# Optimization experiments

Measured on AMD Instinct MI355X. Metric: run time of the kernel, lower is better.

## Reference

```python
import jax, jax.numpy as jnp
import numpy as np

B, D, Nh, L = 8, 128, 8, 1024
Dk = D // Nh  # 16
Dv = D // Nh  # 16

def _xavier(key, shape):
    # nn.init.xavier_normal_ on a 3D tensor treats dim0 as fan irrelevant:
    # fan_in = shape[-1]*1, fan_out = shape[-2]*1 for >=2D; receptive field = prod(shape[2:])? For 3D torch uses
    # fan_in = shape[1]*shape[2]? We just need same distribution family; use std from last two dims.
    fan_in, fan_out = shape[-1], shape[-2]
    std = float(np.sqrt(2.0 / (fan_in + fan_out)))
    return jax.random.normal(key, shape, dtype=jnp.float32) * std

def setup_inputs() -> dict:
    key = jax.random.key(0)
    kx, kq, kk, kv, ko = jax.random.split(key, 5)
    x = jax.random.normal(kx, (B, D, L), dtype=jnp.float32)
    Wq = _xavier(kq, (Nh, B, Dk, D))
    Wk = _xavier(kk, (Nh, B, Dk, D))
    Wv = _xavier(kv, (Nh, B, Dv, D))
    Wo = _xavier(ko, (B, Dv * Nh, D))
    return {"x": x, "Wq": Wq, "Wk": Wk, "Wv": Wv, "Wo": Wo}

def reference(x, Wq, Wk, Wv, Wo):
    scale = 1.0 / np.sqrt(Dk)
    # Project all heads at once: [Nh,B,Dk,D] x [B,D,L] -> [B,Nh,Dk,L]
    Q = jnp.einsum('hbkd,bdl->bhkl', Wq, x)
    K = jnp.einsum('hbkd,bdl->bhkl', Wk, x)
    V = jnp.einsum('hbvd,bdl->bhvl', Wv, x)
    # scores[b,h,i,j] = sum_k Q[b,h,k,i] * K[b,h,k,j]
    scores = jnp.einsum('bhki,bhkj->bhij', Q, K) * scale
    # original softmaxes over dim=1 of [B,L,L] -> the i (Q-length) axis
    attn = jax.nn.softmax(scores, axis=2)
    # head[b,h,v,j] = sum_i V[b,h,v,i] * attn[b,h,i,j]
    head = jnp.einsum('bhvi,bhij->bhvj', V, attn)
    # concat heads along channel dim (order matches torch.cat over head list)
    head = head.reshape(B, Nh * Dv, L)
    # Wo [B, Nh*Dv, D] bmm head [B, D(=Nh*Dv), L] -> [B, Nh*Dv, L]
    out = jnp.einsum('bod,bdl->bol', Wo, head)
    return out
```

## Files before the change

kernel.cpp:

```cpp
#include <hip/hip_runtime.h>
#include <hip/hip_bf16.h>

#define B_ 8
#define D_ 128
#define NH 8
#define L_ 1024
#define DK 16

typedef __attribute__((ext_vector_type(4))) short s4;
typedef __attribute__((ext_vector_type(4))) float f4;

static __device__ __forceinline__ unsigned short f2bf(float f) {
    __hip_bfloat16 h = __float2bfloat16(f);
    return *reinterpret_cast<unsigned short*>(&h);
}
static __device__ __forceinline__ unsigned pack2(float a, float b) {
    return (unsigned)f2bf(a) | ((unsigned)f2bf(b) << 16);
}
static __device__ __forceinline__ s4 pack4(float a, float b, float c, float d) {
    union { unsigned u[2]; s4 v; } un;
    un.u[0] = pack2(a, b);
    un.u[1] = pack2(c, d);
    return un.v;
}

#if __has_builtin(__builtin_amdgcn_mfma_f32_16x16x16_bf16)
#define MFMA16(a, b, c) __builtin_amdgcn_mfma_f32_16x16x16_bf16(a, b, c, 0, 0, 0)
#elif __has_builtin(__builtin_amdgcn_mfma_f32_16x16x16bf16_1k)
#define MFMA16(a, b, c) __builtin_amdgcn_mfma_f32_16x16x16bf16_1k(a, b, c, 0, 0, 0)
#else
static __device__ __forceinline__ f4 mfma16_asm(s4 a, s4 b, f4 c) {
    f4 d;
    asm volatile("v_mfma_f32_16x16x16_bf16 %0, %1, %2, %3"
                 : "=&v"(d) : "v"(a), "v"(b), "v"(c));
    return d;
}
#define MFMA16(a, b, c) mfma16_asm(a, b, c)
#endif

__global__ __launch_bounds__(256)
void proj_kernel(const float* __restrict__ x,
                 const float* __restrict__ Wq,
                 const float* __restrict__ Wk,
                 const float* __restrict__ Wv,
                 unsigned short* __restrict__ Qt,
                 unsigned short* __restrict__ Kt,
                 unsigned short* __restrict__ Vt) {
    const int lane = threadIdx.x & 63;
    const int wv   = threadIdx.x >> 6;
    const int m = lane & 15, q = lane >> 4;
    const int bh = blockIdx.y, b = bh >> 3, h = bh & 7;
    const int which = blockIdx.z;
    const int n0 = (blockIdx.x * 4 + wv) * 32;

    const float* W = (which == 0) ? Wq : (which == 1) ? Wk : Wv;
    const float* Wrow = W + ((size_t)((h * B_ + b) * DK + m)) * D_;
    const float* xb = x + (size_t)b * D_ * L_ + n0 + m;

    f4 acc0 = {0.f, 0.f, 0.f, 0.f}, acc1 = {0.f, 0.f, 0.f, 0.f};
#pragma unroll
    for (int kb = 0; kb < 8; ++kb) {
        const int k4 = kb * 16 + q * 4;
        float4 wf = *(const float4*)(Wrow + k4);
        s4 a = pack4(wf.x, wf.y, wf.z, wf.w);

        const float* xc = xb + (size_t)k4 * L_;
        float b00 = xc[0];          float b01 = xc[L_];
        float b02 = xc[2 * L_];     float b03 = xc[3 * L_];
        float b10 = xc[16];         float b11 = xc[L_ + 16];
        float b12 = xc[2 * L_ + 16];float b13 = xc[3 * L_ + 16];
        s4 bf0 = pack4(b00, b01, b02, b03);
        s4 bf1 = pack4(b10, b11, b12, b13);

        acc0 = MFMA16(a, bf0, acc0);
        acc1 = MFMA16(a, bf1, acc1);
    }

    if (which == 2) {
        unsigned short* vp = Vt + ((size_t)bh * DK + q * 4) * L_ + n0 + m;
        vp[0]      = f2bf(acc0[0]); vp[L_]     = f2bf(acc0[1]);
        vp[2 * L_] = f2bf(acc0[2]); vp[3 * L_] = f2bf(acc0[3]);
        vp += 16;
        vp[0]      = f2bf(acc1[0]); vp[L_]     = f2bf(acc1[1]);
        vp[2 * L_] = f2bf(acc1[2]); vp[3 * L_] = f2bf(acc1[3]);
    } else {
        const float sc = (which == 1) ? 0.25f : 1.0f;
        unsigned short* T = (which == 0) ? Qt : Kt;
        uint2 u0, u1;
        u0.x = pack2(acc0[0] * sc, acc0[1] * sc);
        u0.y = pack2(acc0[2] * sc, acc0[3] * sc);
        u1.x = pack2(acc1[0] * sc, acc1[1] * sc);
        u1.y = pack2(acc1[2] * sc, acc1[3] * sc);
        *(uint2*)(T + ((size_t)bh * L_ + n0 + m) * DK + q * 4)      = u0;
        *(uint2*)(T + ((size_t)bh * L_ + n0 + 16 + m) * DK + q * 4) = u1;
    }
}

__global__ __launch_bounds__(256)
void attn_mfma_kernel(const unsigned short* __restrict__ Qt,
                      const unsigned short* __restrict__ Kt,
                      const unsigned short* __restrict__ Vt,
                      unsigned short* __restrict__ headT) {
    const int lane = threadIdx.x & 63;
    const int wv   = threadIdx.x >> 6;
    const int m    = lane & 15;
    const int q    = lane >> 4;
    const int jt   = blockIdx.x * 4 + wv;
    const int j0   = jt * 16;
    const int bh   = blockIdx.y, b = bh >> 3, h = bh & 7;

    s4 bk = *(const s4*)(Kt + ((size_t)bh * L_ + j0 + m) * DK + q * 4);

    f4 O = {0.f, 0.f, 0.f, 0.f};
    float ls = 0.f;
    const unsigned short* qbase = Qt + (size_t)bh * L_ * DK + q * 4;
    const unsigned short* vbase = Vt + ((size_t)bh * DK + m) * L_ + q * 4;

#pragma unroll 4
    for (int i0 = 0; i0 < L_; i0 += 16) {
        s4 aq = *(const s4*)(qbase + (size_t)(i0 + m) * DK);
        s4 av = *(const s4*)(vbase + i0);

        f4 z = {0.f, 0.f, 0.f, 0.f};
        f4 S = MFMA16(aq, bk, z);

        float p0 = __expf(S[0]), p1 = __expf(S[1]);
        float p2 = __expf(S[2]), p3 = __expf(S[3]);
        ls += (p0 + p1) + (p2 + p3);

        s4 pb;
        pb[0] = (short)f2bf(p0); pb[1] = (short)f2bf(p1);
        pb[2] = (short)f2bf(p2); pb[3] = (short)f2bf(p3);

        O = MFMA16(av, pb, O);
    }

    ls += __shfl_xor(ls, 16, 64);
    ls += __shfl_xor(ls, 32, 64);
    const float inv = 1.f / ls;

    uint2 o;
    o.x = pack2(O[0] * inv, O[1] * inv);
    o.y = pack2(O[2] * inv, O[3] * inv);
    *(uint2*)(headT + ((size_t)b * L_ + j0 + m) * D_ + h * DK + q * 4) = o;
}

__global__ __launch_bounds__(256)
void out_kernel(const unsigned short* __restrict__ headT,
                const float* __restrict__ Wo,
                float* __restrict__ out) {
    const int lane = threadIdx.x & 63;
    const int wv   = threadIdx.x >> 6;
    const int m = lane & 15, q = lane >> 4;
    const int task = blockIdx.x * 4 + wv;
    const int oc = task >> 5;
    const int n0 = (task & 31) * 32;
    const int b  = blockIdx.y;
    const int o0 = oc * 16;

    const float* Wrow = Wo + ((size_t)b * D_ + o0 + m) * D_;
    const unsigned short* h0 = headT + ((size_t)b * L_ + n0 + m) * D_;
    const unsigned short* h1 = h0 + 16 * D_;

    f4 acc0 = {0.f, 0.f, 0.f, 0.f}, acc1 = {0.f, 0.f, 0.f, 0.f};
#pragma unroll
    for (int kb = 0; kb < 8; ++kb) {
        const int k4 = kb * 16 + q * 4;
        float4 wf = *(const float4*)(Wrow + k4);
        s4 a  = pack4(wf.x, wf.y, wf.z, wf.w);
        s4 b0 = *(const s4*)(h0 + k4);
        s4 b1 = *(const s4*)(h1 + k4);
        acc0 = MFMA16(a, b0, acc0);
        acc1 = MFMA16(a, b1, acc1);
    }

    float* op = out + ((size_t)b * D_ + o0 + q * 4) * L_ + n0 + m;
    op[0]      = acc0[0]; op[L_]     = acc0[1];
    op[2 * L_] = acc0[2]; op[3 * L_] = acc0[3];
    op += 16;
    op[0]      = acc1[0]; op[L_]     = acc1[1];
    op[2 * L_] = acc1[2]; op[3 * L_] = acc1[3];
}

extern "C" void kernel_launch(void* const* d_in, const int* in_sizes, int n_in,
                              void* d_out, int out_size, void* d_ws, size_t ws_size,
                              hipStream_t stream) {
    const float* x  = (const float*)d_in[0];
    const float* Wq = (const float*)d_in[1];
    const float* Wk = (const float*)d_in[2];
    const float* Wv = (const float*)d_in[3];
    const float* Wo = (const float*)d_in[4];
    float* out = (float*)d_out;

    const size_t SEG = (size_t)B_ * NH * DK * L_;
    unsigned short* Qt    = (unsigned short*)d_ws;
    unsigned short* Kt    = Qt + SEG;
    unsigned short* Vt    = Kt + SEG;
    unsigned short* headT = Vt + SEG;

    proj_kernel<<<dim3(8, B_ * NH, 3),  256, 0, stream>>>(x, Wq, Wk, Wv, Qt, Kt, Vt);
    attn_mfma_kernel<<<dim3(16, B_ * NH), 256, 0, stream>>>(Qt, Kt, Vt, headT);
    out_kernel <<<dim3(64, B_),         256, 0, stream>>>(headT, Wo, out);
}
```

Before: 119.6 us.

## Fuse attention with output projection via shared-memory head tile

Merges the attention kernel and the output-projection kernel into one kernel. Each block computes a 32-column tile of all eight heads into LDS, then multiplies it by Wo directly, so the headT round trip through global memory and one kernel launch go away. Each wave now handles two heads serially and two key tiles at once, so Q and V loads are reused across the two tiles. The grid drops from 1024 blocks to 256, which leaves about four waves per CU and may hurt latency hiding in the long exp/MFMA loop.

```diff
diff --git a/kernel.cpp b/kernel.cpp
--- a/kernel.cpp
+++ b/kernel.cpp
@@ -97,89 +97,100 @@
 }
 
 __global__ __launch_bounds__(256)
-void attn_mfma_kernel(const unsigned short* __restrict__ Qt,
-                      const unsigned short* __restrict__ Kt,
-                      const unsigned short* __restrict__ Vt,
-                      unsigned short* __restrict__ headT) {
-    const int lane = threadIdx.x & 63;
-    const int wv   = threadIdx.x >> 6;
-    const int m    = lane & 15;
-    const int q    = lane >> 4;
-    const int jt   = blockIdx.x * 4 + wv;
-    const int j0   = jt * 16;
-    const int bh   = blockIdx.y, b = bh >> 3, h = bh & 7;
-
-    s4 bk = *(const s4*)(Kt + ((size_t)bh * L_ + j0 + m) * DK + q * 4);
-
-    f4 O = {0.f, 0.f, 0.f, 0.f};
-    float ls = 0.f;
-    const unsigned short* qbase = Qt + (size_t)bh * L_ * DK + q * 4;
-    const unsigned short* vbase = Vt + ((size_t)bh * DK + m) * L_ + q * 4;
-
-#pragma unroll 4
-    for (int i0 = 0; i0 < L_; i0 += 16) {
-        s4 aq = *(const s4*)(qbase + (size_t)(i0 + m) * DK);
-        s4 av = *(const s4*)(vbase + i0);
-
-        f4 z = {0.f, 0.f, 0.f, 0.f};
-        f4 S = MFMA16(aq, bk, z);
-
-        float p0 = __expf(S[0]), p1 = __expf(S[1]);
-        float p2 = __expf(S[2]), p3 = __expf(S[3]);
-        ls += (p0 + p1) + (p2 + p3);
-
-        s4 pb;
-        pb[0] = (short)f2bf(p0); pb[1] = (short)f2bf(p1);
-        pb[2] = (short)f2bf(p2); pb[3] = (short)f2bf(p3);
-
-        O = MFMA16(av, pb, O);
-    }
-
-    ls += __shfl_xor(ls, 16, 64);
-    ls += __shfl_xor(ls, 32, 64);
-    const float inv = 1.f / ls;
-
-    uint2 o;
-    o.x = pack2(O[0] * inv, O[1] * inv);
-    o.y = pack2(O[2] * inv, O[3] * inv);
-    *(uint2*)(headT + ((size_t)b * L_ + j0 + m) * D_ + h * DK + q * 4) = o;
-}
-
-__global__ __launch_bounds__(256)
-void out_kernel(const unsigned short* __restrict__ headT,
-                const float* __restrict__ Wo,
-                float* __restrict__ out) {
+void attn_out_kernel(const unsigned short* __restrict__ Qt,
+                     const unsigned short* __restrict__ Kt,
+                     const unsigned short* __restrict__ Vt,
+                     const float* __restrict__ Wo,
+                     float* __restrict__ out) {
     const int lane = threadIdx.x & 63;
     const int wv   = threadIdx.x >> 6;
     const int m = lane & 15, q = lane >> 4;
-    const int task = blockIdx.x * 4 + wv;
-    const int oc = task >> 5;
-    const int n0 = (task & 31) * 32;
-    const int b  = blockIdx.y;
-    const int o0 = oc * 16;
-
-    const float* Wrow = Wo + ((size_t)b * D_ + o0 + m) * D_;
-    const unsigned short* h0 = headT + ((size_t)b * L_ + n0 + m) * D_;
-    const unsigned short* h1 = h0 + 16 * D_;
-
-    f4 acc0 = {0.f, 0.f, 0.f, 0.f}, acc1 = {0.f, 0.f, 0.f, 0.f};
-#pragma unroll
-    for (int kb = 0; kb < 8; ++kb) {
-        const int k4 = kb * 16 + q * 4;
-        float4 wf = *(const float4*)(Wrow + k4);
-        s4 a  = pack4(wf.x, wf.y, wf.z, wf.w);
-        s4 b0 = *(const s4*)(h0 + k4);
-        s4 b1 = *(const s4*)(h1 + k4);
-        acc0 = MFMA16(a, b0, acc0);
-        acc1 = MFMA16(a, b1, acc1);
-    }
-
-    float* op = out + ((size_t)b * D_ + o0 + q * 4) * L_ + n0 + m;
-    op[0]      = acc0[0]; op[L_]     = acc0[1];
-    op[2 * L_] = acc0[2]; op[3 * L_] = acc0[3];
-    op += 16;
-    op[0]      = acc1[0]; op[L_]     = acc1[1];
-    op[2 * L_] = acc1[2]; op[3 * L_] = acc1[3];
+    const int b    = blockIdx.y;
+    const int jblk = blockIdx.x * 32;
+
+    __shared__ unsigned short hls[32][132];
+
+#pragma unroll
+    for (int hh = 0; hh < 2; ++hh) {
+        const int h  = wv + hh * 4;
+        const int bh = b * NH + h;
+
+        s4 bk0 = *(const s4*)(Kt + ((size_t)bh * L_ + jblk + m) * DK + q * 4);
+        s4 bk1 = *(const s4*)(Kt + ((size_t)bh * L_ + jblk + 16 + m) * DK + q * 4);
+
+        f4 O0 = {0.f, 0.f, 0.f, 0.f}, O1 = {0.f, 0.f, 0.f, 0.f};
+        float ls0 = 0.f, ls1 = 0.f;
+        const unsigned short* qbase = Qt + (size_t)bh * L_ * DK + q * 4;
+        const unsigned short* vbase = Vt + ((size_t)bh * DK + m) * L_ + q * 4;
+
+#pragma unroll 4
+        for (int i0 = 0; i0 < L_; i0 += 16) {
+            s4 aq = *(const s4*)(qbase + (size_t)(i0 + m) * DK);
+            s4 av = *(const s4*)(vbase + i0);
+
+            f4 z = {0.f, 0.f, 0.f, 0.f};
+            f4 S0 = MFMA16(aq, bk0, z);
+            f4 S1 = MFMA16(aq, bk1, z);
+
+            float p00 = __expf(S0[0]), p01 = __expf(S0[1]);
+            float p02 = __expf(S0[2]), p03 = __expf(S0[3]);
+            float p10 = __expf(S1[0]), p11 = __expf(S1[1]);
+            float p12 = __expf(S1[2]), p13 = __expf(S1[3]);
+            ls0 += (p00 + p01) + (p02 + p03);
+            ls1 += (p10 + p11) + (p12 + p13);
+
+            s4 pb0, pb1;
+            pb0[0] = (short)f2bf(p00); pb0[1] = (short)f2bf(p01);
+            pb0[2] = (short)f2bf(p02); pb0[3] = (short)f2bf(p03);
+            pb1[0] = (short)f2bf(p10); pb1[1] = (short)f2bf(p11);
+            pb1[2] = (short)f2bf(p12); pb1[3] = (short)f2bf(p13);
+
+            O0 = MFMA16(av, pb0, O0);
+            O1 = MFMA16(av, pb1, O1);
+        }
+
+        ls0 += __shfl_xor(ls0, 16, 64);
+        ls0 += __shfl_xor(ls0, 32, 64);
+        ls1 += __shfl_xor(ls1, 16, 64);
+        ls1 += __shfl_xor(ls1, 32, 64);
+        const float inv0 = 1.f / ls0, inv1 = 1.f / ls1;
+
+        uint2 o0, o1;
+        o0.x = pack2(O0[0] * inv0, O0[1] * inv0);
+        o0.y = pack2(O0[2] * inv0, O0[3] * inv0);
+        o1.x = pack2(O1[0] * inv1, O1[1] * inv1);
+        o1.y = pack2(O1[2] * inv1, O1[3] * inv1);
+        *(uint2*)&hls[m][h * 16 + q * 4]      = o0;
+        *(uint2*)&hls[16 + m][h * 16 + q * 4] = o1;
+    }
+
+    __syncthreads();
+
+#pragma unroll
+    for (int t = 0; t < 2; ++t) {
+        const int oc = wv * 2 + t;
+        const int o0 = oc * 16;
+        const float* Wrow = Wo + ((size_t)b * D_ + o0 + m) * D_;
+
+        f4 acc0 = {0.f, 0.f, 0.f, 0.f}, acc1 = {0.f, 0.f, 0.f, 0.f};
+#pragma unroll
+        for (int kb = 0; kb < 8; ++kb) {
+            const int k4 = kb * 16 + q * 4;
+            float4 wf = *(const float4*)(Wrow + k4);
+            s4 a  = pack4(wf.x, wf.y, wf.z, wf.w);
+            s4 b0 = *(const s4*)&hls[m][k4];
+            s4 b1 = *(const s4*)&hls[16 + m][k4];
+            acc0 = MFMA16(a, b0, acc0);
+            acc1 = MFMA16(a, b1, acc1);
+        }
+
+        float* op = out + ((size_t)b * D_ + o0 + q * 4) * L_ + jblk + m;
+        op[0]      = acc0[0]; op[L_]     = acc0[1];
+        op[2 * L_] = acc0[2]; op[3 * L_] = acc0[3];
+        op += 16;
+        op[0]      = acc1[0]; op[L_]     = acc1[1];
+        op[2 * L_] = acc1[2]; op[3 * L_] = acc1[3];
+    }
 }
 
 extern "C" void kernel_launch(void* const* d_in, const int* in_sizes, int n_in,
@@ -193,12 +204,10 @@
     float* out = (float*)d_out;
 
     const size_t SEG = (size_t)B_ * NH * DK * L_;
-    unsigned short* Qt    = (unsigned short*)d_ws;
-    unsigned short* Kt    = Qt + SEG;
-    unsigned short* Vt    = Kt + SEG;
-    unsigned short* headT = Vt + SEG;
-
-    proj_kernel<<<dim3(8, B_ * NH, 3),  256, 0, stream>>>(x, Wq, Wk, Wv, Qt, Kt, Vt);
-    attn_mfma_kernel<<<dim3(16, B_ * NH), 256, 0, stream>>>(Qt, Kt, Vt, headT);
-    out_kernel <<<dim3(64, B_),         256, 0, stream>>>(headT, Wo, out);
-}
+    unsigned short* Qt = (unsigned short*)d_ws;
+    unsigned short* Kt = Qt + SEG;
+    unsigned short* Vt = Kt + SEG;
+
+    proj_kernel<<<dim3(8, B_ * NH, 3), 256, 0, stream>>>(x, Wq, Wk, Wv, Qt, Kt, Vt);
+    attn_out_kernel<<<dim3(32, B_), 256, 0, stream>>>(Qt, Kt, Vt, Wo, out);
+}
```

After: 103.6 us. 1.15x faster.
